# Optimization experiments

Measured on AMD Instinct MI355X. Metric: run time of the kernel, lower is better.

## Reference

```python
import jax, jax.numpy as jnp
import numpy as np

B, T, C = 4, 1024, 1024
H, KV, D = 16, 8, 64   # n_head, kv_heads, dim_head
L = 32                 # partial rotary dim (freqs.shape[-1])
QK_NORM_SCALE = 10.0


def l2norm(t):
    # F.normalize(t, dim=-1): divide by L2 norm clamped to eps
    n = jnp.linalg.norm(t, axis=-1, keepdims=True)
    return t / jnp.maximum(n, 1e-12)


def rotate_half(x):
    # lucidrains rotary: interleaved pairs (d r) with r=2 -> (-x2, x1)
    x1, x2 = x[..., 0::2], x[..., 1::2]
    return jnp.stack((-x2, x1), axis=-1).reshape(x.shape)


def apply_rope(t, freqs):
    # xpos_scale is None in this config -> scale = 1.0
    return t * jnp.cos(freqs) + rotate_half(t) * jnp.sin(freqs)


def setup_inputs() -> dict:
    key = jax.random.key(0)
    ks = jax.random.split(key, 10)
    x = jax.random.normal(ks[0], (B, T, C), dtype=jnp.float32)
    encoded_data = jax.random.normal(ks[1], (B, T, C), dtype=jnp.float32)
    # rotary freqs: positions x inverse frequencies, duplicated interleaved to length L
    pos = jnp.arange(T, dtype=jnp.float32)
    inv_freq = 10000.0 ** (-jnp.arange(L // 2, dtype=jnp.float32) / (L // 2))
    freqs = jnp.repeat(pos[:, None] * inv_freq[None, :], 2, axis=-1)  # (T, L)
    attn_bias = jax.random.normal(ks[2], (H, T, T), dtype=jnp.float32) * 0.02
    Wq = jax.random.normal(ks[3], (C, H * D), dtype=jnp.float32) * 0.02
    Wk = jax.random.normal(ks[4], (C, KV * D), dtype=jnp.float32) * 0.02
    Wv = jax.random.normal(ks[5], (C, KV * D), dtype=jnp.float32) * 0.02
    Wo = jax.random.normal(ks[6], (H * D, C), dtype=jnp.float32) * 0.02
    q_scale = jnp.ones((D,), dtype=jnp.float32)
    k_scale = jnp.ones((D,), dtype=jnp.float32)
    return {"x": x, "encoded_data": encoded_data, "freqs": freqs,
            "attn_bias": attn_bias, "Wq": Wq, "Wk": Wk, "Wv": Wv, "Wo": Wo,
            "q_scale": q_scale, "k_scale": k_scale}


def reference(x, encoded_data, freqs, attn_bias, Wq, Wk, Wv, Wo, q_scale, k_scale):
    Bx, Tx, Cx = x.shape
    q = (x @ Wq).reshape(Bx, Tx, H, D).transpose(0, 2, 1, 3)            # (B,H,T,D)
    k = (encoded_data @ Wk).reshape(Bx, Tx, KV, D).transpose(0, 2, 1, 3)  # (B,KV,T,D)
    v = (encoded_data @ Wv).reshape(Bx, Tx, KV, D).transpose(0, 2, 1, 3)

    # qk-norm
    q = l2norm(q) * q_scale
    k = l2norm(k) * k_scale

    # partial rotary on first L dims (v too, as in the original code)
    l = freqs.shape[-1]
    ql, qr = q[..., :l], q[..., l:]
    kl, kr = k[..., :l], k[..., l:]
    vl, vr = v[..., :l], v[..., l:]
    q = jnp.concatenate([apply_rope(ql, freqs), qr], axis=-1)
    k = jnp.concatenate([apply_rope(kl, freqs), kr], axis=-1)
    v = jnp.concatenate([apply_rope(vl, freqs), vr], axis=-1)

    # GQA: k,v repeated along head dim (KV -> H = 2*KV)
    k = jnp.tile(k, (1, 2, 1, 1))
    v = jnp.tile(v, (1, 2, 1, 1))

    # pre-scale q, then SDPA applies its own default D^-0.5 (faithful to source)
    default_scale = D ** (-0.5)
    q = q * (default_scale / QK_NORM_SCALE)

    mask_value = -jnp.finfo(q.dtype).max
    causal = jnp.triu(jnp.ones((Tx, Tx), dtype=bool), k=1)  # j > i masked
    bias = jnp.where(causal, mask_value / 2, attn_bias)      # (H,T,T)

    scores = jnp.einsum('bhqd,bhkd->bhqk', q, k) * default_scale + bias[None]
    attn = jax.nn.softmax(scores, axis=-1)
    y = jnp.einsum('bhqk,bhkd->bhqd', attn, v)                # (B,H,T,D)
    y = y.transpose(0, 2, 1, 3).reshape(Bx, Tx, H * D)
    return y @ Wo
```

## Files before the change

### kernel.cpp

```cpp
#include <hip/hip_runtime.h>

typedef unsigned short u16;
typedef __attribute__((ext_vector_type(8))) __bf16 bf16x8;
typedef __attribute__((ext_vector_type(4))) float f32x4;
typedef __attribute__((ext_vector_type(16))) float f32x16;

#define LOG2E 1.44269504088896f

__device__ __forceinline__ u16 f2bf(float f) {
  union { float f; unsigned u; } c; c.f = f;
  unsigned u = c.u;
  return (u16)((u + 0x7fffu + ((u >> 16) & 1u)) >> 16);
}
__device__ __forceinline__ float bf2f(u16 h) {
  union { unsigned u; float f; } c; c.u = ((unsigned)h) << 16;
  return c.f;
}

__device__ __forceinline__ void load_lds16(const void* g, void* l) {
  __builtin_amdgcn_global_load_lds((const __attribute__((address_space(1))) unsigned int*)g,
                                   (__attribute__((address_space(3))) unsigned int*)l, 16, 0, 0);
}

__global__ void prologue_kernel(const float* __restrict__ x, const float* __restrict__ enc,
                                const float* __restrict__ freqs,
                                const float* __restrict__ Wq, const float* __restrict__ Wk,
                                const float* __restrict__ Wv, const float* __restrict__ Wo,
                                u16* __restrict__ xb, u16* __restrict__ eb,
                                u16* __restrict__ WqT, u16* __restrict__ WkT,
                                u16* __restrict__ WvT, u16* __restrict__ WoT,
                                float* __restrict__ cstab, float* __restrict__ sntab) {
  __shared__ float tile[32][33];
  int id = blockIdx.x;
  int tid = threadIdx.x;
  if (id < 2048) {
    const int n4each = 1048576;
    int stride = 2048 * 256;
    for (int i = id * 256 + tid; i < 2 * n4each; i += stride) {
      const float4* src; ushort4* dst; int j;
      if (i < n4each) { src = (const float4*)x; dst = (ushort4*)xb; j = i; }
      else            { src = (const float4*)enc; dst = (ushort4*)eb; j = i - n4each; }
      float4 v = src[j];
      ushort4 o;
      o.x = f2bf(v.x); o.y = f2bf(v.y); o.z = f2bf(v.z); o.w = f2bf(v.w);
      dst[j] = o;
    }
    return;
  }
  if (id < 2176) {
    int i = (id - 2048) * 256 + tid;
    float f = freqs[i];
    float sn, cs;
    sincosf(f, &sn, &cs);
    cstab[i] = cs; sntab[i] = sn;
    return;
  }
  int rem = id - 2176;
  int z = rem >> 10;
  int ry = (rem >> 5) & 31;
  int rx = rem & 31;
  const float* in; u16* out; int C;
  if (z == 0)      { in = Wq; out = WqT; C = 1024; }
  else if (z == 1) { in = Wk; out = WkT; C = 512; }
  else if (z == 2) { in = Wv; out = WvT; C = 512; }
  else             { in = Wo; out = WoT; C = 1024; }
  const int R = 1024;
  int c0 = rx * 32, r0 = ry * 32;
  if (c0 >= C) return;
  int tx = tid & 31, ty = tid >> 5;
#pragma unroll
  for (int i = 0; i < 4; ++i)
    tile[ty + 8 * i][tx] = in[(size_t)(r0 + ty + 8 * i) * C + c0 + tx];
  __syncthreads();
#pragma unroll
  for (int i = 0; i < 4; ++i)
    out[(size_t)(c0 + ty + 8 * i) * R + r0 + tx] = f2bf(tile[tx][ty + 8 * i]);
}

__device__ __forceinline__ void gemm_bn64_core(const u16* A, const u16* Bt, int K,
                                               u16* As, u16* Bs, f32x4 (&acc)[2][4]) {
  int tid = threadIdx.x;
  int w = tid >> 6, l = tid & 63;
  int g = l >> 4, lr = l & 15;
  int m0 = blockIdx.x * 128, n0 = blockIdx.y * 64;
#pragma unroll
  for (int m = 0; m < 2; ++m)
#pragma unroll
    for (int n = 0; n < 4; ++n) acc[m][n] = (f32x4){0.f, 0.f, 0.f, 0.f};

  for (int k0 = 0; k0 < K; k0 += 64) {
#pragma unroll
    for (int rnd = 0; rnd < 4; ++rnd) {
      int bidx = rnd * 4096 + w * 1024 + l * 16;
      int row = bidx >> 7, colb = bidx & 127;
      int scol = colb ^ ((row & 7) << 4);
      load_lds16((const char*)A + ((size_t)(m0 + row) * K + k0) * 2 + scol,
                 (char*)As + rnd * 4096 + w * 1024);
    }
#pragma unroll
    for (int rnd = 0; rnd < 2; ++rnd) {
      int bidx = rnd * 4096 + w * 1024 + l * 16;
      int row = bidx >> 7, colb = bidx & 127;
      int scol = colb ^ ((row & 7) << 4);
      load_lds16((const char*)Bt + ((size_t)(n0 + row) * K + k0) * 2 + scol,
                 (char*)Bs + rnd * 4096 + w * 1024);
    }
    __syncthreads();
    bf16x8 af[2][2], bfr[4][2];
#pragma unroll
    for (int m = 0; m < 2; ++m) {
      int ra = w * 32 + m * 16 + lr;
#pragma unroll
      for (int kf = 0; kf < 2; ++kf)
        af[m][kf] = *(const bf16x8*)((const char*)As + ra * 128 + ((kf * 64 + g * 16) ^ ((ra & 7) << 4)));
    }
#pragma unroll
    for (int n = 0; n < 4; ++n) {
      int rb = n * 16 + lr;
#pragma unroll
      for (int kf = 0; kf < 2; ++kf)
        bfr[n][kf] = *(const bf16x8*)((const char*)Bs + rb * 128 + ((kf * 64 + g * 16) ^ ((rb & 7) << 4)));
    }
#pragma unroll
    for (int m = 0; m < 2; ++m)
#pragma unroll
      for (int n = 0; n < 4; ++n) {
        acc[m][n] = __builtin_amdgcn_mfma_f32_16x16x32_bf16(af[m][0], bfr[n][0], acc[m][n], 0, 0, 0);
        acc[m][n] = __builtin_amdgcn_mfma_f32_16x16x32_bf16(af[m][1], bfr[n][1], acc[m][n], 0, 0, 0);
      }
    __syncthreads();
  }
}

__global__ __launch_bounds__(256, 4) void gemm_qkv_kernel(const u16* xb, const u16* eb,
                                                          const u16* WqT, const u16* WkT, const u16* WvT,
                                                          const float* __restrict__ qscale,
                                                          const float* __restrict__ kscale,
                                                          const float* __restrict__ cstab,
                                                          const float* __restrict__ sntab,
                                                          const float* __restrict__ bias,
                                                          u16* Qb, u16* Ktiles, u16* Vtiles,
                                                          u16* __restrict__ biasTT) {
  __shared__ __align__(16) char sh[24576];
  u16* As = (u16*)sh;
  u16* Bs = (u16*)(sh + 16384);
  int z = blockIdx.z;
  const u16* A; const u16* Bt; int N;
  if (z == 0)      { A = xb; Bt = WqT; N = 1024; }
  else if (z == 1) { A = eb; Bt = WkT; N = 512; }
  else             { A = eb; Bt = WvT; N = 512; }

  if ((int)blockIdx.y * 64 >= N) {
    int flat = (z - 1) * 256 + ((int)blockIdx.y - 8) * 32 + (int)blockIdx.x;
    int w = threadIdx.x >> 6, lane = threadIdx.x & 63;
    float* lt = (float*)(sh + w * 4224);
    int ql = lane & 31, hi = lane >> 5;
    for (int f = flat * 4 + w; f < 8448; f += 2048) {
      int h = f / 528, rem = f - h * 528;
      int qt = (int)((sqrtf(8.f * (float)rem + 1.f) - 1.f) * 0.5f);
      while ((qt + 1) * (qt + 2) / 2 <= rem) ++qt;
      while (qt * (qt + 1) / 2 > rem) --qt;
      int kt = rem - qt * (qt + 1) / 2;
      const float* tsrc = bias + ((size_t)h * 1024 + qt * 32) * 1024 + kt * 32;
#pragma unroll
      for (int i = 0; i < 4; ++i) {
        int row = i * 8 + (lane >> 3);
        int c4 = (lane & 7) * 4;
        float4 v4 = *(const float4*)(tsrc + (size_t)row * 1024 + c4);
        lt[row * 33 + c4 + 0] = v4.x; lt[row * 33 + c4 + 1] = v4.y;
        lt[row * 33 + c4 + 2] = v4.z; lt[row * 33 + c4 + 3] = v4.w;
      }
      u16 v[16];
#pragma unroll
      for (int r = 0; r < 16; ++r) {
        int c = (r & 3) + 8 * (r >> 2) + 4 * hi;
        v[r] = f2bf(lt[ql * 33 + c] * LOG2E);
      }
      u16* dst = biasTT + (size_t)f * 1024 + lane * 16;
#pragma unroll
      for (int i = 0; i < 4; ++i) {
        ushort4 o; o.x = v[i * 4]; o.y = v[i * 4 + 1]; o.z = v[i * 4 + 2]; o.w = v[i * 4 + 3];
        *(ushort4*)(dst + i * 4) = o;
      }
    }
    return;
  }

  f32x4 acc[2][4];
  gemm_bn64_core(A, Bt, 1024, As, Bs, acc);

  int tid = threadIdx.x;
  int w = tid >> 6, l = tid & 63;
  int g = l >> 4, lr = l & 15;
  int m0 = blockIdx.x * 128, n0 = blockIdx.y * 64;
  int head = n0 >> 6;

  if (z == 2) {
#pragma unroll
    for (int m = 0; m < 2; ++m) {
      int rowb = m0 + w * 32 + m * 16 + g * 4;
#pragma unroll
      for (int r = 0; r < 4; ++r) {
        int row = rowb + r;
        int t = row & 1023, b = row >> 10;
        char* tbase = (char*)Vtiles + (size_t)((b * 8 + head) * 32 + (t >> 5)) * 4096;
        int kb = (t & 31) * 2;
#pragma unroll
        for (int n = 0; n < 4; ++n) {
          int dloc = n * 16 + lr;
          float v = acc[m][n][r];
          if (n < 2) {
            float cs = cstab[t * 32 + dloc];
            float sn = sntab[t * 32 + dloc];
            float partner = __shfl_xor(v, 1);
            float rot = (lr & 1) ? partner : -partner;
            v = v * cs + rot * sn;
          }
          int rr = dloc & 31;
          int scol = ((dloc >> 5) << 6) | kb;
          *(u16*)(tbase + rr * 128 + (scol ^ ((rr & 7) << 4))) = f2bf(v);
        }
      }
    }
    return;
  }

  const float* scale = (z == 0) ? qscale : kscale;
  float fs = (z == 0) ? 0.0015625f * LOG2E : 1.0f;
#pragma unroll
  for (int m = 0; m < 2; ++m) {
    int rowb = m0 + w * 32 + m * 16 + g * 4;
#pragma unroll
    for (int r = 0; r < 4; ++r) {
      int row = rowb + r;
      int t = row & 1023, b = row >> 10;
      float ss = 0.f;
#pragma unroll
      for (int n = 0; n < 4; ++n) { float v = acc[m][n][r]; ss += v * v; }
#pragma unroll
      for (int d = 1; d < 16; d <<= 1) ss += __shfl_xor(ss, d);
      float inv = 1.0f / fmaxf(sqrtf(ss), 1e-12f);
#pragma unroll
      for (int n = 0; n < 4; ++n) {
        int dloc = n * 16 + lr;
        float v = acc[m][n][r] * inv * scale[dloc];
        if (n < 2) {
          float cs = cstab[t * 32 + dloc];
          float sn = sntab[t * 32 + dloc];
          float partner = __shfl_xor(v, 1);
          float rot = (lr & 1) ? partner : -partner;
          v = v * cs + rot * sn;
        }
        v *= fs;
        if (z == 0) {
          Qb[((size_t)(b * 16 + head) * 1024 + t) * 64 + dloc] = f2bf(v);
        } else {
          int tile = (b * 8 + head) * 32 + (t >> 5);
          int rin = t & 31;
          *(u16*)((char*)Ktiles + (size_t)tile * 4096 + rin * 128 + ((dloc * 2) ^ ((rin & 7) << 4))) = f2bf(v);
        }
      }
    }
  }
}

__global__ __launch_bounds__(256, 4) void gemm_out_kernel(const u16* Yb, const u16* WoT, float* out) {
  __shared__ __align__(16) u16 As[128 * 64];
  __shared__ __align__(16) u16 Bs[64 * 64];
  f32x4 acc[2][4];
  gemm_bn64_core(Yb, WoT, 1024, As, Bs, acc);
  int tid = threadIdx.x;
  int w = tid >> 6, l = tid & 63;
  int g = l >> 4, lr = l & 15;
  int m0 = blockIdx.x * 128, n0 = blockIdx.y * 64;
#pragma unroll
  for (int m = 0; m < 2; ++m)
#pragma unroll
    for (int n = 0; n < 4; ++n) {
      int row = m0 + w * 32 + m * 16 + g * 4;
      int col = n0 + n * 16 + lr;
#pragma unroll
      for (int r = 0; r < 4; ++r)
        out[(size_t)(row + r) * 1024 + col] = acc[m][n][r];
    }
}

__device__ __forceinline__ unsigned pack_bf2(float lo, float hi_) {
  union { __bf16 h[2]; unsigned u; } c;
  c.h[0] = (__bf16)lo; c.h[1] = (__bf16)hi_;
  return c.u;
}

__global__ __launch_bounds__(256, 4) void attn_kernel(const u16* __restrict__ Qb, const u16* __restrict__ Ktiles,
                                                      const u16* __restrict__ Vtiles, const u16* __restrict__ biasTT,
                                                      u16* __restrict__ Yb) {
  __shared__ __align__(16) char smem[33280];
  int tid = threadIdx.x;
  int w = tid >> 6;
  int lane = tid & 63;
  int ql = lane & 31;
  int hi = lane >> 5;
  int id = blockIdx.x;
  int xcd = id & 7;
  int j = id >> 3;
  int b = j & 3;
  int gslot = j >> 2;
  int g = gslot * 8 + xcd;
  int h = g & 15;
  int qt = 31 - (g >> 4);
  int kv = h & 7;
  int qg = qt * 32 + ql;
  int nt = qt + 1;

  char* stg = smem + w * 8192;

  const u16* Qrow = Qb + ((size_t)(b * 16 + h) * 1024 + qg) * 64;
  bf16x8 qf[4];
#pragma unroll
  for (int ks = 0; ks < 4; ++ks) qf[ks] = *(const bf16x8*)(Qrow + ks * 16 + hi * 8);

  const char* Ktb = (const char*)Ktiles + (size_t)((b * 8 + kv) * 32) * 4096;
  const char* Vtb = (const char*)Vtiles + (size_t)((b * 8 + kv) * 32) * 4096;
  const u16* btb = biasTT + (size_t)(h * 528 + qt * (qt + 1) / 2) * 1024;

  f32x16 o0, o1;
#pragma unroll
  for (int r = 0; r < 16; ++r) { o0[r] = 0.f; o1[r] = 0.f; }
  float lsum = 0.f;

  for (int it = w; it < nt; it += 4) {
    int t0 = it * 32;
    const char* Ksrc = Ktb + (size_t)it * 4096 + lane * 16;
    const char* Vsrc = Vtb + (size_t)it * 4096 + lane * 16;
#pragma unroll
    for (int i = 0; i < 4; ++i) load_lds16(Ksrc + i * 1024, stg + i * 1024);
#pragma unroll
    for (int i = 0; i < 4; ++i) load_lds16(Vsrc + i * 1024, stg + 4096 + i * 1024);
    __builtin_amdgcn_sched_barrier(0);
    asm volatile("s_waitcnt vmcnt(4)" ::: "memory");
    __builtin_amdgcn_sched_barrier(0);
    const u16* bl = btb + (size_t)it * 1024 + lane * 16;
    bf16x8 ba = *(const bf16x8*)bl;
    bf16x8 bb2 = *(const bf16x8*)(bl + 8);
    f32x16 s;
#pragma unroll
    for (int r = 0; r < 16; ++r) s[r] = 0.f;
#pragma unroll
    for (int ks = 0; ks < 4; ++ks) {
      bf16x8 kc = *(const bf16x8*)(stg + ql * 128 + ((ks * 32 + hi * 16) ^ ((ql & 7) << 4)));
      s = __builtin_amdgcn_mfma_f32_32x32x16_bf16(kc, qf[ks], s, 0, 0, 0);
    }
    bool diag = (it == nt - 1);
    float p[16];
    float ssum = 0.f;
#pragma unroll
    for (int r = 0; r < 16; ++r) {
      float sv = s[r] + (float)(r < 8 ? ba[r & 7] : bb2[r & 7]);
      if (diag) {
        int key = t0 + (r & 3) + 8 * (r >> 2) + 4 * hi;
        if (key > qg) sv = -1e30f;
      }
      float pe = exp2f(sv);
      p[r] = pe;
      ssum += pe;
    }
    lsum += ssum;
    unsigned pk[8], tk[8];
#pragma unroll
    for (int j2 = 0; j2 < 8; ++j2) pk[j2] = pack_bf2(p[2 * j2], p[2 * j2 + 1]);
#pragma unroll
    for (int j2 = 0; j2 < 8; ++j2) tk[j2] = (unsigned)__shfl_xor((int)pk[j2], 32);
    union PU { unsigned u[4]; bf16x8 v; };
    PU pb0, pb1;
    pb0.u[0] = hi ? tk[2] : pk[0];
    pb0.u[1] = hi ? tk[3] : pk[1];
    pb0.u[2] = hi ? pk[2] : tk[0];
    pb0.u[3] = hi ? pk[3] : tk[1];
    pb1.u[0] = hi ? tk[6] : pk[4];
    pb1.u[1] = hi ? tk[7] : pk[5];
    pb1.u[2] = hi ? pk[6] : tk[4];
    pb1.u[3] = hi ? pk[7] : tk[5];
    asm volatile("s_waitcnt vmcnt(0)" ::: "memory");
    __builtin_amdgcn_sched_barrier(0);
    char* Vl = stg + 4096;
    bf16x8 v00 = *(const bf16x8*)(Vl + ql * 128 + (((0 << 6) | (0 * 32 + hi * 16)) ^ ((ql & 7) << 4)));
    bf16x8 v01 = *(const bf16x8*)(Vl + ql * 128 + (((0 << 6) | (1 * 32 + hi * 16)) ^ ((ql & 7) << 4)));
    bf16x8 v10 = *(const bf16x8*)(Vl + ql * 128 + (((1 << 6) | (0 * 32 + hi * 16)) ^ ((ql & 7) << 4)));
    bf16x8 v11 = *(const bf16x8*)(Vl + ql * 128 + (((1 << 6) | (1 * 32 + hi * 16)) ^ ((ql & 7) << 4)));
    o0 = __builtin_amdgcn_mfma_f32_32x32x16_bf16(v00, pb0.v, o0, 0, 0, 0);
    o0 = __builtin_amdgcn_mfma_f32_32x32x16_bf16(v01, pb1.v, o0, 0, 0, 0);
    o1 = __builtin_amdgcn_mfma_f32_32x32x16_bf16(v10, pb0.v, o1, 0, 0, 0);
    o1 = __builtin_amdgcn_mfma_f32_32x32x16_bf16(v11, pb1.v, o1, 0, 0, 0);
  }

  lsum += __shfl_xor(lsum, 32);
  u16* Osh = (u16*)stg;
  float* Lsh = (float*)(smem + 32768);
#pragma unroll
  for (int r = 0; r < 16; ++r) {
    int row = (r & 3) + 8 * (r >> 2) + 4 * hi;
    Osh[row * 32 + ql]        = f2bf(o0[r]);
    Osh[(row + 32) * 32 + ql] = f2bf(o1[r]);
  }
  if (hi == 0) Lsh[w * 32 + ql] = lsum;
  __syncthreads();

  {
    int q = tid & 31, dg = tid >> 5;
    float* Lsh2 = (float*)(smem + 32768);
    float ltot = Lsh2[q] + Lsh2[32 + q] + Lsh2[64 + q] + Lsh2[96 + q];
    float invl = 1.0f / ltot;
    u16 ov[8];
#pragma unroll
    for (int j2 = 0; j2 < 8; ++j2) {
      int d = dg * 8 + j2;
      float acc = bf2f(*(u16*)(smem + 0 * 8192 + (d * 32 + q) * 2)) +
                  bf2f(*(u16*)(smem + 1 * 8192 + (d * 32 + q) * 2)) +
                  bf2f(*(u16*)(smem + 2 * 8192 + (d * 32 + q) * 2)) +
                  bf2f(*(u16*)(smem + 3 * 8192 + (d * 32 + q) * 2));
      ov[j2] = f2bf(acc * invl);
    }
    ushort4 out0, out1;
    out0.x = ov[0]; out0.y = ov[1]; out0.z = ov[2]; out0.w = ov[3];
    out1.x = ov[4]; out1.y = ov[5]; out1.z = ov[6]; out1.w = ov[7];
    u16* Yp = Yb + ((size_t)b * 1024 + qt * 32 + q) * 1024 + h * 64 + dg * 8;
    *(ushort4*)Yp = out0;
    *(ushort4*)(Yp + 4) = out1;
  }
}

extern "C" void kernel_launch(void* const* d_in, const int* in_sizes, int n_in,
                              void* d_out, int out_size, void* d_ws, size_t ws_size,
                              hipStream_t stream) {
  const float* x     = (const float*)d_in[0];
  const float* enc   = (const float*)d_in[1];
  const float* freqs = (const float*)d_in[2];
  const float* bias  = (const float*)d_in[3];
  const float* Wq    = (const float*)d_in[4];
  const float* Wk    = (const float*)d_in[5];
  const float* Wv    = (const float*)d_in[6];
  const float* Wo    = (const float*)d_in[7];
  const float* qs    = (const float*)d_in[8];
  const float* ks    = (const float*)d_in[9];

  char* ws = (char*)d_ws;
  size_t off = 0;
  auto alloc = [&](size_t bytes) { char* p = ws + off; off += (bytes + 255) & ~(size_t)255; return p; };
  u16*   xb     = (u16*)alloc(8388608);
  u16*   eb     = (u16*)alloc(8388608);
  u16*   WqT    = (u16*)alloc(2097152);
  u16*   WkT    = (u16*)alloc(1048576);
  u16*   WvT    = (u16*)alloc(1048576);
  u16*   WoT    = (u16*)alloc(2097152);
  u16*   Qb     = (u16*)alloc(8388608);
  u16*   Ktiles = (u16*)alloc(4194304);
  u16*   Vtiles = (u16*)alloc(4194304);
  u16*   biasTT = (u16*)alloc(17301504);
  float* cstab  = (float*)alloc(131072);
  float* sntab  = (float*)alloc(131072);
  u16*   Yb     = (u16*)xb;

  prologue_kernel<<<6272, 256, 0, stream>>>(x, enc, freqs, Wq, Wk, Wv, Wo,
                                            xb, eb, WqT, WkT, WvT, WoT, cstab, sntab);

  gemm_qkv_kernel<<<dim3(32, 16, 3), 256, 0, stream>>>(xb, eb, WqT, WkT, WvT,
                                                       qs, ks, cstab, sntab, bias,
                                                       Qb, Ktiles, Vtiles, biasTT);

  attn_kernel<<<dim3(2048), 256, 0, stream>>>(Qb, Ktiles, Vtiles, biasTT, Yb);

  gemm_out_kernel<<<dim3(32, 16), 256, 0, stream>>>(Yb, WoT, (float*)d_out);
}
```

Before: 88.84 us.

## Double-buffer GEMM LDS tiles and interleave bias-transpose blocks with QKV GEMM blocks

The shared GEMM core now double-buffers its LDS tiles, issuing global-to-LDS loads for the next K-slice before computing on the current one, so memory latency overlaps with the MFMA work. Each k-step also drops one of its two barriers. The QKV kernel moves to a flat 1-D grid in which every third block does the bias-tile conversion and the other two do GEMM tiles, so memory-bound and compute-bound work run at the same time instead of the bias blocks trailing the launch order. In exchange, LDS use doubles to 48KB and launch bounds drop to 3 blocks per SM, which lowers occupancy. A single barrier per step may also leave a write-after-read race on the buffer being refilled.

Measured after the change: 92.60 us. +4.2%, slower.

```diff
diff --git a/kernel.cpp b/kernel.cpp
--- a/kernel.cpp
+++ b/kernel.cpp
@@ -77,25 +77,26 @@
     out[(size_t)(c0 + ty + 8 * i) * R + r0 + tx] = f2bf(tile[tx][ty + 8 * i]);
 }
 
-__device__ __forceinline__ void gemm_bn64_core(const u16* A, const u16* Bt, int K,
-                                               u16* As, u16* Bs, f32x4 (&acc)[2][4]) {
+__device__ __forceinline__ void gemm_bn64_dbuf(const u16* A, const u16* Bt, int K,
+                                               char* sh, int m0, int n0, f32x4 (&acc)[2][4]) {
   int tid = threadIdx.x;
   int w = tid >> 6, l = tid & 63;
   int g = l >> 4, lr = l & 15;
-  int m0 = blockIdx.x * 128, n0 = blockIdx.y * 64;
 #pragma unroll
   for (int m = 0; m < 2; ++m)
 #pragma unroll
     for (int n = 0; n < 4; ++n) acc[m][n] = (f32x4){0.f, 0.f, 0.f, 0.f};
 
-  for (int k0 = 0; k0 < K; k0 += 64) {
+  auto stage = [&](int buf, int k0) {
+    char* As = sh + buf * 24576;
+    char* Bs = As + 16384;
 #pragma unroll
     for (int rnd = 0; rnd < 4; ++rnd) {
       int bidx = rnd * 4096 + w * 1024 + l * 16;
       int row = bidx >> 7, colb = bidx & 127;
       int scol = colb ^ ((row & 7) << 4);
       load_lds16((const char*)A + ((size_t)(m0 + row) * K + k0) * 2 + scol,
-                 (char*)As + rnd * 4096 + w * 1024);
+                 As + rnd * 4096 + w * 1024);
     }
 #pragma unroll
     for (int rnd = 0; rnd < 2; ++rnd) {
@@ -103,23 +104,32 @@
       int row = bidx >> 7, colb = bidx & 127;
       int scol = colb ^ ((row & 7) << 4);
       load_lds16((const char*)Bt + ((size_t)(n0 + row) * K + k0) * 2 + scol,
-                 (char*)Bs + rnd * 4096 + w * 1024);
-    }
-    __syncthreads();
+                 Bs + rnd * 4096 + w * 1024);
+    }
+  };
+
+  stage(0, 0);
+  __syncthreads();
+  int nk = K >> 6;
+  for (int ki = 0; ki < nk; ++ki) {
+    int cur = ki & 1;
+    if (ki + 1 < nk) stage(cur ^ 1, (ki + 1) << 6);
+    const char* As = sh + cur * 24576;
+    const char* Bs = As + 16384;
     bf16x8 af[2][2], bfr[4][2];
 #pragma unroll
     for (int m = 0; m < 2; ++m) {
       int ra = w * 32 + m * 16 + lr;
 #pragma unroll
       for (int kf = 0; kf < 2; ++kf)
-        af[m][kf] = *(const bf16x8*)((const char*)As + ra * 128 + ((kf * 64 + g * 16) ^ ((ra & 7) << 4)));
+        af[m][kf] = *(const bf16x8*)(As + ra * 128 + ((kf * 64 + g * 16) ^ ((ra & 7) << 4)));
     }
 #pragma unroll
     for (int n = 0; n < 4; ++n) {
       int rb = n * 16 + lr;
 #pragma unroll
       for (int kf = 0; kf < 2; ++kf)
-        bfr[n][kf] = *(const bf16x8*)((const char*)Bs + rb * 128 + ((kf * 64 + g * 16) ^ ((rb & 7) << 4)));
+        bfr[n][kf] = *(const bf16x8*)(Bs + rb * 128 + ((kf * 64 + g * 16) ^ ((rb & 7) << 4)));
     }
 #pragma unroll
     for (int m = 0; m < 2; ++m)
@@ -132,7 +142,7 @@
   }
 }
 
-__global__ __launch_bounds__(256, 4) void gemm_qkv_kernel(const u16* xb, const u16* eb,
+__global__ __launch_bounds__(256, 3) void gemm_qkv_kernel(const u16* xb, const u16* eb,
                                                           const u16* WqT, const u16* WkT, const u16* WvT,
                                                           const float* __restrict__ qscale,
                                                           const float* __restrict__ kscale,
@@ -141,17 +151,11 @@
                                                           const float* __restrict__ bias,
                                                           u16* Qb, u16* Ktiles, u16* Vtiles,
                                                           u16* __restrict__ biasTT) {
-  __shared__ __align__(16) char sh[24576];
-  u16* As = (u16*)sh;
-  u16* Bs = (u16*)(sh + 16384);
-  int z = blockIdx.z;
-  const u16* A; const u16* Bt; int N;
-  if (z == 0)      { A = xb; Bt = WqT; N = 1024; }
-  else if (z == 1) { A = eb; Bt = WkT; N = 512; }
-  else             { A = eb; Bt = WvT; N = 512; }
-
-  if ((int)blockIdx.y * 64 >= N) {
-    int flat = (z - 1) * 256 + ((int)blockIdx.y - 8) * 32 + (int)blockIdx.x;
+  __shared__ __align__(16) char sh[49152];
+  int id = blockIdx.x;
+  int sel = id % 3;
+  if (sel == 2) {
+    int flat = id / 3;
     int w = threadIdx.x >> 6, lane = threadIdx.x & 63;
     float* lt = (float*)(sh + w * 4224);
     int ql = lane & 31, hi = lane >> 5;
@@ -185,14 +189,25 @@
     }
     return;
   }
+  int gi = (id / 3) * 2 + sel;
+  int xblk = gi & 31;
+  int t = gi >> 5;
+  int z, y;
+  if (t < 16)      { z = 0; y = t; }
+  else if (t < 24) { z = 1; y = t - 16; }
+  else             { z = 2; y = t - 24; }
+  const u16* A; const u16* Bt;
+  if (z == 0)      { A = xb; Bt = WqT; }
+  else if (z == 1) { A = eb; Bt = WkT; }
+  else             { A = eb; Bt = WvT; }
+  int m0 = xblk * 128, n0 = y * 64;
 
   f32x4 acc[2][4];
-  gemm_bn64_core(A, Bt, 1024, As, Bs, acc);
+  gemm_bn64_dbuf(A, Bt, 1024, sh, m0, n0, acc);
 
   int tid = threadIdx.x;
   int w = tid >> 6, l = tid & 63;
   int g = l >> 4, lr = l & 15;
-  int m0 = blockIdx.x * 128, n0 = blockIdx.y * 64;
   int head = n0 >> 6;
 
   if (z == 2) {
@@ -202,16 +217,16 @@
 #pragma unroll
       for (int r = 0; r < 4; ++r) {
         int row = rowb + r;
-        int t = row & 1023, b = row >> 10;
-        char* tbase = (char*)Vtiles + (size_t)((b * 8 + head) * 32 + (t >> 5)) * 4096;
-        int kb = (t & 31) * 2;
+        int t2 = row & 1023, b = row >> 10;
+        char* tbase = (char*)Vtiles + (size_t)((b * 8 + head) * 32 + (t2 >> 5)) * 4096;
+        int kb = (t2 & 31) * 2;
 #pragma unroll
         for (int n = 0; n < 4; ++n) {
           int dloc = n * 16 + lr;
           float v = acc[m][n][r];
           if (n < 2) {
-            float cs = cstab[t * 32 + dloc];
-            float sn = sntab[t * 32 + dloc];
+            float cs = cstab[t2 * 32 + dloc];
+            float sn = sntab[t2 * 32 + dloc];
             float partner = __shfl_xor(v, 1);
             float rot = (lr & 1) ? partner : -partner;
             v = v * cs + rot * sn;
@@ -233,7 +248,7 @@
 #pragma unroll
     for (int r = 0; r < 4; ++r) {
       int row = rowb + r;
-      int t = row & 1023, b = row >> 10;
+      int t2 = row & 1023, b = row >> 10;
       float ss = 0.f;
 #pragma unroll
       for (int n = 0; n < 4; ++n) { float v = acc[m][n][r]; ss += v * v; }
@@ -245,18 +260,18 @@
         int dloc = n * 16 + lr;
         float v = acc[m][n][r] * inv * scale[dloc];
         if (n < 2) {
-          float cs = cstab[t * 32 + dloc];
-          float sn = sntab[t * 32 + dloc];
+          float cs = cstab[t2 * 32 + dloc];
+          float sn = sntab[t2 * 32 + dloc];
           float partner = __shfl_xor(v, 1);
           float rot = (lr & 1) ? partner : -partner;
           v = v * cs + rot * sn;
         }
         v *= fs;
         if (z == 0) {
-          Qb[((size_t)(b * 16 + head) * 1024 + t) * 64 + dloc] = f2bf(v);
+          Qb[((size_t)(b * 16 + head) * 1024 + t2) * 64 + dloc] = f2bf(v);
         } else {
-          int tile = (b * 8 + head) * 32 + (t >> 5);
-          int rin = t & 31;
+          int tile = (b * 8 + head) * 32 + (t2 >> 5);
+          int rin = t2 & 31;
           *(u16*)((char*)Ktiles + (size_t)tile * 4096 + rin * 128 + ((dloc * 2) ^ ((rin & 7) << 4))) = f2bf(v);
         }
       }
@@ -264,15 +279,15 @@
   }
 }
 
-__global__ __launch_bounds__(256, 4) void gemm_out_kernel(const u16* Yb, const u16* WoT, float* out) {
-  __shared__ __align__(16) u16 As[128 * 64];
-  __shared__ __align__(16) u16 Bs[64 * 64];
+__global__ __launch_bounds__(256, 3) void gemm_out_kernel(const u16* Yb, const u16* WoT, float* out) {
+  __shared__ __align__(16) char sh[49152];
+  int id = blockIdx.x;
+  int m0 = (id & 31) * 128, n0 = (id >> 5) * 64;
   f32x4 acc[2][4];
-  gemm_bn64_core(Yb, WoT, 1024, As, Bs, acc);
+  gemm_bn64_dbuf(Yb, WoT, 1024, sh, m0, n0, acc);
   int tid = threadIdx.x;
   int w = tid >> 6, l = tid & 63;
   int g = l >> 4, lr = l & 15;
-  int m0 = blockIdx.x * 128, n0 = blockIdx.y * 64;
 #pragma unroll
   for (int m = 0; m < 2; ++m)
 #pragma unroll
@@ -463,11 +478,11 @@
   prologue_kernel<<<6272, 256, 0, stream>>>(x, enc, freqs, Wq, Wk, Wv, Wo,
                                             xb, eb, WqT, WkT, WvT, WoT, cstab, sntab);
 
-  gemm_qkv_kernel<<<dim3(32, 16, 3), 256, 0, stream>>>(xb, eb, WqT, WkT, WvT,
-                                                       qs, ks, cstab, sntab, bias,
-                                                       Qb, Ktiles, Vtiles, biasTT);
+  gemm_qkv_kernel<<<1536, 256, 0, stream>>>(xb, eb, WqT, WkT, WvT,
+                                            qs, ks, cstab, sntab, bias,
+                                            Qb, Ktiles, Vtiles, biasTT);
 
   attn_kernel<<<dim3(2048), 256, 0, stream>>>(Qb, Ktiles, Vtiles, biasTT, Yb);
 
-  gemm_out_kernel<<<dim3(32, 16), 256, 0, stream>>>(Yb, WoT, (float*)d_out);
-}
+  gemm_out_kernel<<<512, 256, 0, stream>>>(Yb, WoT, (float*)d_out);
+}
```
